# Optimization experiments

Measured on AMD Instinct MI355X. Metric: run time of the kernel, lower is better.

Reference implementation:

```python
import jax, jax.numpy as jnp
import numpy as np

DT = 0.05
T_STEPS = 100  # arange(0, 5, 0.05)


def setup_inputs() -> dict:
    key = jax.random.key(0)
    k1, k2, k3 = jax.random.split(key, 3)
    batch, dim = 256, 64
    initial_position = jax.random.normal(k1, (batch, dim), dtype=jnp.float32)
    # scale W down so dynamics stay bounded over the integration horizon
    W = jax.random.normal(k2, (dim, dim), dtype=jnp.float32) / jnp.sqrt(dim).astype(jnp.float32)
    b = jax.random.normal(k3, (dim,), dtype=jnp.float32) * 0.1
    return {"initial_position": initial_position, "W": W, "b": b}


def reference(initial_position, W, b):
    dim = W.shape[0]
    I = jnp.eye(dim, dtype=initial_position.dtype)
    expm_b = jax.vmap(jax.scipy.linalg.expm)  # batched matrix exponential

    def step(x, _):
        # x: (B, D). Regime mask from pre-activation z = x @ W^T + b.
        z = x @ W.T + b
        m = (z > 0).astype(x.dtype)                    # (B, D)
        W_eff = m[:, :, None] * W[None, :, :]          # rows of W scaled by mask
        b_eff = m * b                                  # (B, D)
        A = W_eff - I                                  # (B, D, D)
        A_exp = expm_b(A * DT)                         # (B, D, D)
        A_inv = jnp.linalg.pinv(A)                     # (B, D, D)
        Ainv_b = jnp.einsum('bij,bj->bi', A_inv, b_eff)
        B_term = jnp.einsum('bij,bj->bi', A_exp - I, Ainv_b)
        x_next = jnp.einsum('bij,bj->bi', A_exp, x) + B_term
        return x_next, x  # trajectory stores state BEFORE the update

    _, traj = jax.lax.scan(step, initial_position, None, length=T_STEPS)
    # traj: (T, B, D) -> (B, T, D)
    return jnp.transpose(traj, (1, 0, 2))
```

## Files before the change

kernel.cpp:

```cpp
#include <hip/hip_runtime.h>


#define DT_F 0.05f
#define T_STEPS 100
#define DD 64
#define KT 3

__device__ __forceinline__ float matvec64(const float (&Wr)[DD], float w) {
    const int wi = __float_as_int(w);
    float a0 = 0.f, a1 = 0.f, a2 = 0.f, a3 = 0.f;
#pragma unroll
    for (int j = 0; j < DD; j += 4) {
        const float s0 = __int_as_float(__builtin_amdgcn_readlane(wi, j + 0));
        const float s1 = __int_as_float(__builtin_amdgcn_readlane(wi, j + 1));
        const float s2 = __int_as_float(__builtin_amdgcn_readlane(wi, j + 2));
        const float s3 = __int_as_float(__builtin_amdgcn_readlane(wi, j + 3));
        a0 = fmaf(Wr[j + 0], s0, a0);
        a1 = fmaf(Wr[j + 1], s1, a1);
        a2 = fmaf(Wr[j + 2], s2, a2);
        a3 = fmaf(Wr[j + 3], s3, a3);
    }
    return (a0 + a1) + (a2 + a3);
}

__global__ __launch_bounds__(64, 1)
void abla_kernel(const float* __restrict__ x0,
                 const float* __restrict__ W,
                 const float* __restrict__ bvec,
                 float* __restrict__ out) {
    const int batch = blockIdx.x;
    const int lane = threadIdx.x;

    float Wr[DD];
#pragma unroll
    for (int j = 0; j < DD; j += 4) {
        const float4 w4 = *reinterpret_cast<const float4*>(W + lane * DD + j);
        Wr[j + 0] = w4.x; Wr[j + 1] = w4.y; Wr[j + 2] = w4.z; Wr[j + 3] = w4.w;
    }
    const float bi = bvec[lane];
    float x = x0[batch * DD + lane];
    float* outp = out + (size_t)batch * T_STEPS * DD + lane;

    for (int t = 0; t < T_STEPS; ++t) {
        outp[(size_t)t * DD] = x;

        const float z = matvec64(Wr, x) + bi;
        const float m_dt = (z > 0.f) ? DT_F : 0.f;
        float w = m_dt * z - DT_F * x;
        float y = x + w;

#pragma unroll
        for (int k = 2; k <= KT; ++k) {
            const float v = matvec64(Wr, w);
            w = (m_dt * v - DT_F * w) * (1.0f / (float)k);
            y += w;
        }
        x = y;
    }
}

extern "C" void kernel_launch(void* const* d_in, const int* in_sizes, int n_in,
                              void* d_out, int out_size, void* d_ws, size_t ws_size,
                              hipStream_t stream) {
    const float* x0 = (const float*)d_in[0];
    const float* W  = (const float*)d_in[1];
    const float* b  = (const float*)d_in[2];
    float* out = (float*)d_out;

    const int batch = in_sizes[0] / DD;
    abla_kernel<<<batch, DD, 0, stream>>>(x0, W, b, out);
}
```

Before: 118.6 us.

## Broadcast vector via LDS float4 reads and use packed FMA in matvec

Replaces per-element readlane broadcasts with a write of each lane's value to shared memory followed by float4 broadcast loads, and accumulates with 2-wide packed FMAs (v_pk_fma_f32) over W rows held as float2 pairs. It ping-pongs between two LDS buffers so no barrier is needed within a single wave. The goal is to cut the 64 scalar readlane instructions and halve the FMA count per matvec. The cost is LDS latency on the serial dependency chain, and it relies on single-wave execution for correctness without syncs.

```diff
diff --git a/kernel.cpp b/kernel.cpp
--- a/kernel.cpp
+++ b/kernel.cpp
@@ -6,24 +6,31 @@
 #define DD 64
 #define KT 3
 
-__device__ __forceinline__ float matvec64(const float (&Wr)[DD], float w) {
-    const int wi = __float_as_int(w);
-    float a0 = 0.f, a1 = 0.f, a2 = 0.f, a3 = 0.f;
+typedef float v2f __attribute__((ext_vector_type(2)));
+
+__device__ __forceinline__ float matvec64(const v2f (&Wp)[32], float w,
+                                          float4* __restrict__ s4, int lane) {
+    reinterpret_cast<float*>(s4)[lane] = w;
+
+    v2f acc0 = {0.f, 0.f}, acc1 = {0.f, 0.f};
+    v2f acc2 = {0.f, 0.f}, acc3 = {0.f, 0.f};
 #pragma unroll
-    for (int j = 0; j < DD; j += 4) {
-        const float s0 = __int_as_float(__builtin_amdgcn_readlane(wi, j + 0));
-        const float s1 = __int_as_float(__builtin_amdgcn_readlane(wi, j + 1));
-        const float s2 = __int_as_float(__builtin_amdgcn_readlane(wi, j + 2));
-        const float s3 = __int_as_float(__builtin_amdgcn_readlane(wi, j + 3));
-        a0 = fmaf(Wr[j + 0], s0, a0);
-        a1 = fmaf(Wr[j + 1], s1, a1);
-        a2 = fmaf(Wr[j + 2], s2, a2);
-        a3 = fmaf(Wr[j + 3], s3, a3);
+    for (int r = 0; r < 16; r += 2) {
+        const float4 qa = s4[r + 0];
+        const float4 qb = s4[r + 1];
+        const v2f sa0 = {qa.x, qa.y}, sa1 = {qa.z, qa.w};
+        const v2f sb0 = {qb.x, qb.y}, sb1 = {qb.z, qb.w};
+        acc0 = __builtin_elementwise_fma(Wp[2 * r + 0], sa0, acc0);
+        acc1 = __builtin_elementwise_fma(Wp[2 * r + 1], sa1, acc1);
+        acc2 = __builtin_elementwise_fma(Wp[2 * r + 2], sb0, acc2);
+        acc3 = __builtin_elementwise_fma(Wp[2 * r + 3], sb1, acc3);
     }
-    return (a0 + a1) + (a2 + a3);
+    const v2f ps = (acc0 + acc1) + (acc2 + acc3);
+    return ps.x + ps.y;
 }
 
 __global__ __launch_bounds__(64, 1)
+__attribute__((amdgpu_waves_per_eu(1, 1)))
 void abla_kernel(const float* __restrict__ x0,
                  const float* __restrict__ W,
                  const float* __restrict__ bvec,
@@ -31,31 +38,46 @@
     const int batch = blockIdx.x;
     const int lane = threadIdx.x;
 
-    float Wr[DD];
+    __shared__ float4 sbuf[2][DD / 4];
+
+    v2f Wp[32];
 #pragma unroll
     for (int j = 0; j < DD; j += 4) {
         const float4 w4 = *reinterpret_cast<const float4*>(W + lane * DD + j);
-        Wr[j + 0] = w4.x; Wr[j + 1] = w4.y; Wr[j + 2] = w4.z; Wr[j + 3] = w4.w;
+        Wp[j / 2 + 0] = v2f{w4.x, w4.y};
+        Wp[j / 2 + 1] = v2f{w4.z, w4.w};
     }
+#pragma unroll
+    for (int p = 0; p < 32; ++p)
+        asm("" : "+v"(Wp[p]));
+
     const float bi = bvec[lane];
     float x = x0[batch * DD + lane];
     float* outp = out + (size_t)batch * T_STEPS * DD + lane;
 
+    float4* sA = &sbuf[0][0];
+    float4* sB = &sbuf[1][0];
+
     for (int t = 0; t < T_STEPS; ++t) {
         outp[(size_t)t * DD] = x;
 
-        const float z = matvec64(Wr, x) + bi;
+        const float z = matvec64(Wp, x, sA, lane) + bi;
         const float m_dt = (z > 0.f) ? DT_F : 0.f;
         float w = m_dt * z - DT_F * x;
         float y = x + w;
 
-#pragma unroll
-        for (int k = 2; k <= KT; ++k) {
-            const float v = matvec64(Wr, w);
-            w = (m_dt * v - DT_F * w) * (1.0f / (float)k);
+        {
+            const float v = matvec64(Wp, w, sB, lane);
+            w = (m_dt * v - DT_F * w) * 0.5f;
+            y += w;
+        }
+        {
+            const float v = matvec64(Wp, w, sA, lane);
+            w = (m_dt * v - DT_F * w) * (1.0f / 3.0f);
             y += w;
         }
         x = y;
+        float4* tmp = sA; sA = sB; sB = tmp;
     }
 }
 
```

Measured after the change: 143.9 us. 1.21x slower.
